# Optimization experiments

Hardware: AMD Instinct MI355X
Metric: run time of the kernel (lower is better)

The kernel has to match this reference:

```python
import jax, jax.numpy as jnp
import numpy as np

NX, NU, N, BATCH = 64, 32, 32, 192
NEWTON_ITERS = 2  # fixed outer Newton iterations (original loops to kkt_tol)


def setup_inputs() -> dict:
    key = jax.random.key(0)
    ks = jax.random.split(key, 8)
    x0 = jax.random.normal(ks[0], (BATCH, NX), jnp.float32)
    x = 0.1 * jax.random.normal(ks[1], (N + 1, BATCH, NX), jnp.float32)
    u = 0.1 * jax.random.normal(ks[2], (N, BATCH, NU), jnp.float32)
    lmd = jnp.zeros((N + 1, BATCH, NX), jnp.float32)
    # linear dynamics x+ = A x + Bm u (stable-ish A)
    A = 0.9 * jnp.eye(NX, dtype=jnp.float32) + (0.1 / np.sqrt(NX)) * jax.random.normal(ks[3], (NX, NX), jnp.float32)
    Bm = jax.random.normal(ks[4], (NX, NU), jnp.float32) / np.sqrt(NX)
    # quadratic cost weights (symmetric PD)
    Cx = jax.random.normal(ks[5], (NX, NX), jnp.float32) / np.sqrt(NX)
    Qx = Cx @ Cx.T + 0.1 * jnp.eye(NX, dtype=jnp.float32)
    Cu = jax.random.normal(ks[6], (NU, NU), jnp.float32) / np.sqrt(NU)
    Ru = Cu @ Cu.T + jnp.eye(NU, dtype=jnp.float32)
    Cf = jax.random.normal(ks[7], (NX, NX), jnp.float32) / np.sqrt(NX)
    Qf = Cf @ Cf.T + 0.1 * jnp.eye(NX, dtype=jnp.float32)
    return {"x0": x0, "x": x, "u": u, "lmd": lmd, "A": A, "Bm": Bm, "Qx": Qx, "Ru": Ru, "Qf": Qf}


def _eval_kkt(x0, x, u, lmd, A, Bm, Qx, Ru, Qf):
    # KKT residuals of the LQ OCP (GaussNewton; vectorized over stages s and batch b)
    x0res = x[0] - x0                                                   # [B,nx]
    xs = x[:-1]                                                         # [N,B,nx]
    xres = jnp.einsum('ij,sbj->sbi', A, xs) + jnp.einsum('ij,sbj->sbi', Bm, u) - x[1:]
    lx = jnp.einsum('ij,sbj->sbi', Qx, xs) + jnp.einsum('ji,sbj->sbi', A, lmd[1:]) - lmd[:-1]
    lu = jnp.einsum('ij,sbj->sbi', Ru, u) + jnp.einsum('ji,sbj->sbi', Bm, lmd[1:])
    lxN = jnp.einsum('ij,bj->bi', Qf, x[-1]) - lmd[-1]                  # terminal gradient residual
    return x0res, xres, lx, lu, lxN


def _riccati(x0res, xres, lx, lu, lxN, A, Bm, Qx, Ru, Qf):
    B_, nx = x0res.shape
    PN = jnp.broadcast_to(Qf, (B_, nx, nx))

    def bwd(carry, inp):
        P, p = carry
        lx_i, lu_i, xres_i = inp
        PA = jnp.einsum('bij,jk->bik', P, A)
        PB = jnp.einsum('bij,jk->bik', P, Bm)
        Qxx = Qx[None] + jnp.einsum('ji,bjk->bik', A, PA)
        Quu = Ru[None] + jnp.einsum('ji,bjk->bik', Bm, PB)
        Qxu = jnp.einsum('ji,bjk->bik', A, PB)
        w = jnp.einsum('bij,bj->bi', P, xres_i) + p
        qx = lx_i + jnp.einsum('ji,bj->bi', A, w)
        qu = lu_i + jnp.einsum('ji,bj->bi', Bm, w)
        rhs = jnp.concatenate([jnp.swapaxes(Qxu, 1, 2), qu[..., None]], axis=2)
        sol = -jnp.linalg.solve(Quu, rhs)
        K, k = sol[..., :nx], sol[..., nx]
        Pn = Qxx + jnp.einsum('bxi,biy->bxy', Qxu, K)
        Pn = 0.5 * (Pn + jnp.swapaxes(Pn, 1, 2))
        pn = qx + jnp.einsum('bxi,bi->bx', Qxu, k)
        return (Pn, pn), (Pn, pn, K, k)

    (_, _), (Ps, ps, Ks, ks) = jax.lax.scan(bwd, (PN, lxN), (lx, lu, xres), reverse=True)
    Ps = jnp.concatenate([Ps, PN[None]], axis=0)   # [N+1,B,nx,nx]
    ps = jnp.concatenate([ps, lxN[None]], axis=0)  # [N+1,B,nx]

    def fwd(dx, inp):
        K, k, xres_i = inp
        du = jnp.einsum('bux,bx->bu', K, dx) + k
        dxn = jnp.einsum('ij,bj->bi', A, dx) + jnp.einsum('ij,bj->bi', Bm, du) + xres_i
        return dxn, (dx, du)

    dxN, (dxs, dus) = jax.lax.scan(fwd, -x0res, (Ks, ks, xres))
    dxs = jnp.concatenate([dxs, dxN[None]], axis=0)
    dlmd = jnp.einsum('sbij,sbj->sbi', Ps, dxs) + ps
    return dxs, dus, dlmd


def _solve(x0, x, u, lmd, A, Bm, Qx, Ru, Qf):
    for _ in range(NEWTON_ITERS):
        x0res, xres, lx, lu, lxN = _eval_kkt(x0, x, u, lmd, A, Bm, Qx, Ru, Qf)
        dx, du, dlmd = _riccati(x0res, xres, lx, lu, lxN, A, Bm, Qx, Ru, Qf)
        x = x + dx
        u = u + du
        lmd = lmd + dlmd
    return x, u, lmd


def reference(x0, x, u, lmd, A, Bm, Qx, Ru, Qf):
    # returns the optimized control trajectory u* [N,B,nu]
    return _solve(x0, x, u, lmd, A, Bm, Qx, Ru, Qf)[1]
```

## Files before the change

### kernel.cpp

```cpp
#include <hip/hip_runtime.h>

#define DEV __device__ __forceinline__

constexpr int NX = 64, NU = 32, NH = 32, NB = 192;

constexpr int WS_P  = 0;
constexpr int WS_QI = WS_P  + (NH + 1) * NX * NX;
constexpr int WS_X  = WS_QI + NH * NU * NU;
constexpr int WS_K  = WS_X  + NH * NX * NU;

typedef __attribute__((ext_vector_type(8))) short bf16x8;
typedef __attribute__((ext_vector_type(4))) float f32x4;
typedef __attribute__((ext_vector_type(4))) unsigned short us4;

constexpr int LVL_M2T = 96 * 72 * 2;
constexpr int LVL_P   = 64 * 72 * 2;
constexpr int LVL_TT  = 96 * 72 * 2;
constexpr int LVL_XU  = 64 * 40 * 2;
constexpr int LVL_KT  = 64 * 40 * 2;
constexpr int LVL_QI  = 32 * 40 * 2;
constexpr int oM2T = 0;
constexpr int oP   = oM2T + 3 * LVL_M2T;
constexpr int oTT  = oP   + 3 * LVL_P;
constexpr int oXU  = oTT  + 3 * LVL_TT;
constexpr int oKT  = oXU  + 2 * LVL_XU;
constexpr int oQI  = oKT  + 2 * LVL_KT;
constexpr int oQXX = oQI  + 2 * LVL_QI;
constexpr int SMEMB = oQXX + 64 * 68 * 4;

DEV unsigned short bfh(float x) {
  unsigned u = __float_as_uint(x);
  return (unsigned short)((u + 0x7FFFu + ((u >> 16) & 1u)) >> 16);
}
DEV float bf2f(unsigned short h) { return __uint_as_float(((unsigned)h) << 16); }
DEV void split3(float x, unsigned short& h, unsigned short& m, unsigned short& l) {
  h = bfh(x); float r1 = x - bf2f(h);
  m = bfh(r1); float r2 = r1 - bf2f(m);
  l = bfh(r2);
}
DEV float4 ld4(const float* p) { return *reinterpret_cast<const float4*>(p); }
DEV void   st4(float* p, float4 v) { *reinterpret_cast<float4*>(p) = v; }
DEV void st4_nt(float* p, f32x4 v) {
  __builtin_nontemporal_store(v, (f32x4*)p);
}
DEV float  dot4(float4 a, float4 b) {
  return fmaf(a.x, b.x, fmaf(a.y, b.y, fmaf(a.z, b.z, a.w * b.w)));
}
DEV void fma4(float4& a, float s, float4 b) {
  a.x = fmaf(s, b.x, a.x); a.y = fmaf(s, b.y, a.y);
  a.z = fmaf(s, b.z, a.z); a.w = fmaf(s, b.w, a.w);
}
DEV void fma8(float* acc, float s, float4 b0, float4 b1) {
  acc[0] = fmaf(s, b0.x, acc[0]); acc[1] = fmaf(s, b0.y, acc[1]);
  acc[2] = fmaf(s, b0.z, acc[2]); acc[3] = fmaf(s, b0.w, acc[3]);
  acc[4] = fmaf(s, b1.x, acc[4]); acc[5] = fmaf(s, b1.y, acc[5]);
  acc[6] = fmaf(s, b1.z, acc[6]); acc[7] = fmaf(s, b1.w, acc[7]);
}

#define MFMA16(a, b, c) __builtin_amdgcn_mfma_f32_16x16x32_bf16(a, b, c, 0, 0, 0)

DEV f32x4 prod33(const char* A, int ao, int LA, const char* B, int bo, int LB,
                 f32x4 acc) {
  const bf16x8 a0 = *(const bf16x8*)(A + ao);
  const bf16x8 a1 = *(const bf16x8*)(A + LA + ao);
  const bf16x8 a2 = *(const bf16x8*)(A + 2 * LA + ao);
  const bf16x8 b0 = *(const bf16x8*)(B + bo);
  const bf16x8 b1 = *(const bf16x8*)(B + LB + bo);
  const bf16x8 b2 = *(const bf16x8*)(B + 2 * LB + bo);
  acc = MFMA16(a1, b1, acc);
  acc = MFMA16(a2, b0, acc);
  acc = MFMA16(a0, b2, acc);
  acc = MFMA16(a1, b0, acc);
  acc = MFMA16(a0, b1, acc);
  acc = MFMA16(a0, b0, acc);
  return acc;
}
DEV f32x4 prod22(const char* A, int ao, int LA, const char* B, int bo, int LB,
                 f32x4 acc) {
  const bf16x8 a0 = *(const bf16x8*)(A + ao);
  const bf16x8 a1 = *(const bf16x8*)(A + LA + ao);
  const bf16x8 b0 = *(const bf16x8*)(B + bo);
  const bf16x8 b1 = *(const bf16x8*)(B + LB + bo);
  acc = MFMA16(a1, b0, acc);
  acc = MFMA16(a0, b1, acc);
  acc = MFMA16(a0, b0, acc);
  return acc;
}
DEV void st_pack3(char* base, int lvl, int el, f32x4 v) {
  us4 h, m, l;
#pragma unroll
  for (int r = 0; r < 4; ++r) {
    unsigned short hh, mm, ll; split3(v[r], hh, mm, ll);
    h[r] = (short)hh; m[r] = (short)mm; l[r] = (short)ll;
  }
  *(us4*)(base + el * 2) = h;
  *(us4*)(base + lvl + el * 2) = m;
  *(us4*)(base + 2 * lvl + el * 2) = l;
}
DEV void st_pack2(char* base, int lvl, int el, f32x4 v) {
  us4 h, l;
#pragma unroll
  for (int r = 0; r < 4; ++r) {
    const unsigned short hh = bfh(v[r]);
    h[r] = (short)hh;
    l[r] = (short)bfh(v[r] - bf2f(hh));
  }
  *(us4*)(base + el * 2) = h;
  *(us4*)(base + lvl + el * 2) = l;
}

DEV void producer(char* smem, const float* Ag, const float* Bg,
                  const float* Qxg, const float* Rug, const float* Qfg,
                  float* ws) {
  const int t = threadIdx.x, lane = t & 63, wv = t >> 6;
  const int l15 = lane & 15, l4 = lane >> 4;

  char* M2T = smem + oM2T;
  char* Pp  = smem + oP;
  char* TT  = smem + oTT;
  char* XU  = smem + oXU;
  char* KT  = smem + oKT;
  char* QI  = smem + oQI;
  float* QXX = (float*)(smem + oQXX);
  float* QUU = (float*)(smem + oQXX);

  float* gP  = ws + WS_P;
  float* gQI = ws + WS_QI;
  float* gX  = ws + WS_X;
  float* gK  = ws + WS_K;
  int* flags = (int*)(ws + WS_P);

  for (int idx = t; idx < 96 * 64; idx += 512) {
    const int j = idx >> 6, m = idx & 63;
    const float v = (j < 64) ? Ag[m * 64 + j] : Bg[m * 32 + (j - 64)];
    unsigned short h, mi, lo; split3(v, h, mi, lo);
    const int eo = (j * 72 + m) * 2;
    *(unsigned short*)(M2T + eo) = h;
    *(unsigned short*)(M2T + LVL_M2T + eo) = mi;
    *(unsigned short*)(M2T + 2 * LVL_M2T + eo) = lo;
  }
  for (int idx = t; idx < 64 * 64; idx += 512) {
    const int r = idx >> 6, c = idx & 63;
    const float v = Qfg[idx];
    unsigned short h, mi, lo; split3(v, h, mi, lo);
    const int eo = (r * 72 + c) * 2;
    *(unsigned short*)(Pp + eo) = h;
    *(unsigned short*)(Pp + LVL_P + eo) = mi;
    *(unsigned short*)(Pp + 2 * LVL_P + eo) = lo;
    __builtin_nontemporal_store(v, gP + 32 * 4096 + idx);
  }
  __syncthreads();

  for (int s = NH - 1; s >= 0; --s) {
    {
      const int mT = wv >> 1, jT = 4 + (wv & 1);
      f32x4 acc = {0.f, 0.f, 0.f, 0.f};
#pragma unroll
      for (int kp = 0; kp < 2; ++kp) {
        const int ao = ((mT * 16 + l15) * 72 + kp * 32 + l4 * 8) * 2;
        const int bo = ((jT * 16 + l15) * 72 + kp * 32 + l4 * 8) * 2;
        acc = prod33(Pp, ao, LVL_P, M2T, bo, LVL_M2T, acc);
      }
      st_pack3(TT, LVL_TT, (jT * 16 + l15) * 72 + mT * 16 + l4 * 4, acc);
    }
    __syncthreads();

    if (wv < 4) {
      const int uA = wv >> 1, uB = wv & 1;
      f32x4 acc = {0.f, 0.f, 0.f, 0.f};
#pragma unroll
      for (int kp = 0; kp < 2; ++kp) {
        const int ao = (((4 + uA) * 16 + l15) * 72 + kp * 32 + l4 * 8) * 2;
        const int bo = ((64 + uB * 16 + l15) * 72 + kp * 32 + l4 * 8) * 2;
        acc = prod33(TT, ao, LVL_TT, M2T, bo, LVL_M2T, acc);
      }
      const int c = uB * 16 + l15, u0 = uA * 16 + l4 * 4;
      const float4 rv = ld4(Rug + c * 32 + u0);
      QUU[c * 36 + u0 + 0] = acc[0] + rv.x;
      QUU[c * 36 + u0 + 1] = acc[1] + rv.y;
      QUU[c * 36 + u0 + 2] = acc[2] + rv.z;
      QUU[c * 36 + u0 + 3] = acc[3] + rv.w;
    } else {
      for (int q = wv - 4; q < 8; q += 4) {
        const int uT = q & 1, xT = q >> 1;
        f32x4 acc = {0.f, 0.f, 0.f, 0.f};
#pragma unroll
        for (int kp = 0; kp < 2; ++kp) {
          const int ao = (((4 + uT) * 16 + l15) * 72 + kp * 32 + l4 * 8) * 2;
          const int bo = ((xT * 16 + l15) * 72 + kp * 32 + l4 * 8) * 2;
          acc = prod33(TT, ao, LVL_TT, M2T, bo, LVL_M2T, acc);
        }
        const int x = xT * 16 + l15, u0 = uT * 16 + l4 * 4;
        st_pack2(XU, LVL_XU, x * 40 + u0, acc);
        st4_nt(gX + s * 2048 + x * 32 + u0, acc);
      }
    }
    __syncthreads();

    if (wv == 0) {
      const int i = lane & 31, h = lane >> 5;
      float W[16];
#pragma unroll
      for (int r = 0; r < 16; ++r) W[r] = QUU[i * 36 + h * 16 + r];
#pragma unroll
      for (int j = 0; j < 32; ++j) {
        const int jh = j >> 4, jr = j & 15;
        const float d = __shfl(W[jr], j | (jh << 5));
        const float pinv = 1.0f / d;
        const float f = __shfl(W[jr], i | (jh << 5));
        float pr[16];
#pragma unroll
        for (int r = 0; r < 16; ++r) pr[r] = __shfl(W[r], j | (h << 5));
        float nw[16];
        if (i == j) {
#pragma unroll
          for (int r = 0; r < 16; ++r) nw[r] = pr[r] * pinv;
          if (h == jh) nw[jr] = pinv;
        } else {
          const float g = f * pinv;
#pragma unroll
          for (int r = 0; r < 16; ++r) nw[r] = fmaf(-g, pr[r], W[r]);
          if (h == jh) nw[jr] = -g;
        }
#pragma unroll
        for (int r = 0; r < 16; ++r) W[r] = nw[r];
      }
#pragma unroll
      for (int q = 0; q < 4; ++q) {
        f32x4 o = {W[4 * q], W[4 * q + 1], W[4 * q + 2], W[4 * q + 3]};
        st4_nt(gQI + s * 1024 + i * 32 + h * 16 + 4 * q, o);
        us4 hh, ll;
#pragma unroll
        for (int r = 0; r < 4; ++r) {
          const unsigned short hv = bfh(W[4 * q + r]);
          hh[r] = (short)hv;
          ll[r] = (short)bfh(W[4 * q + r] - bf2f(hv));
        }
        *(us4*)(QI + (i * 40 + h * 16 + 4 * q) * 2) = hh;
        *(us4*)(QI + LVL_QI + (i * 40 + h * 16 + 4 * q) * 2) = ll;
      }
    } else {
      for (int tt = wv - 1; tt < 16; tt += 7) {
        const int mT = tt & 3, jT = tt >> 2;
        f32x4 acc = {0.f, 0.f, 0.f, 0.f};
#pragma unroll
        for (int kp = 0; kp < 2; ++kp) {
          const int ao = ((mT * 16 + l15) * 72 + kp * 32 + l4 * 8) * 2;
          const int bo = ((jT * 16 + l15) * 72 + kp * 32 + l4 * 8) * 2;
          acc = prod33(Pp, ao, LVL_P, M2T, bo, LVL_M2T, acc);
        }
        st_pack3(TT, LVL_TT, (jT * 16 + l15) * 72 + mT * 16 + l4 * 4, acc);
      }
    }
    __syncthreads();

    if (wv < 2) {
      for (int tt = wv; tt < 8; tt += 2) {
        const int mT = tt & 1, xT = tt >> 1;
        f32x4 acc = {0.f, 0.f, 0.f, 0.f};
        const int ao = ((mT * 16 + l15) * 40 + l4 * 8) * 2;
        const int bo = ((xT * 16 + l15) * 40 + l4 * 8) * 2;
        acc = prod22(QI, ao, LVL_QI, XU, bo, LVL_XU, acc);
        const int x = xT * 16 + l15, m0 = mT * 16 + l4 * 4;
#pragma unroll
        for (int r = 0; r < 4; ++r)
          __builtin_nontemporal_store(-acc[r], gK + s * 2048 + (m0 + r) * 64 + x);
        st_pack2(KT, LVL_KT, x * 40 + m0, acc);
      }
    } else {
      for (int tt = wv - 2; tt < 16; tt += 6) {
        const int jT = tt >> 2, iT = tt & 3;
        f32x4 acc = {0.f, 0.f, 0.f, 0.f};
#pragma unroll
        for (int kp = 0; kp < 2; ++kp) {
          const int ao = ((jT * 16 + l15) * 72 + kp * 32 + l4 * 8) * 2;
          const int bo = ((iT * 16 + l15) * 72 + kp * 32 + l4 * 8) * 2;
          acc = prod33(TT, ao, LVL_TT, M2T, bo, LVL_M2T, acc);
        }
        const int c = iT * 16 + l15, j0 = jT * 16 + l4 * 4;
        const float4 q = ld4(Qxg + c * 64 + j0);
        QXX[c * 68 + j0 + 0] = acc[0] + q.x;
        QXX[c * 68 + j0 + 1] = acc[1] + q.y;
        QXX[c * 68 + j0 + 2] = acc[2] + q.z;
        QXX[c * 68 + j0 + 3] = acc[3] + q.w;
      }
    }
    __syncthreads();

    if (t == 0) {
      __threadfence();
      __hip_atomic_store(flags + s, 1, __ATOMIC_RELEASE, __HIP_MEMORY_SCOPE_AGENT);
    }

    if (s > 0) {
      for (int tt = wv; tt < 16; tt += 8) {
        const int iT = tt & 3, jT = tt >> 2;
        f32x4 acc = {0.f, 0.f, 0.f, 0.f};
        const int ao = ((iT * 16 + l15) * 40 + l4 * 8) * 2;
        const int bo = ((jT * 16 + l15) * 40 + l4 * 8) * 2;
        acc = prod22(XU, ao, LVL_XU, KT, bo, LVL_KT, acc);
        const int j = jT * 16 + l15, i0 = iT * 16 + l4 * 4;
        f32x4 pv;
#pragma unroll
        for (int r = 0; r < 4; ++r) {
          pv[r] = QXX[(i0 + r) * 68 + j] - acc[r];
          __builtin_nontemporal_store(pv[r], gP + s * 4096 + (i0 + r) * 64 + j);
        }
        st_pack3(Pp, LVL_P, j * 72 + i0, pv);
      }
    }
    __syncthreads();
  }
}

DEV void consumer(float* lds, int b, const float* x0g, const float* xg,
                  const float* ug, const float* lg, const float* Ag,
                  const float* Bg, const float* Qxg, const float* Rug,
                  const float* Qfg, float* ws, float* outp) {
  const int t = threadIdx.x;
  const float* gP  = ws + WS_P;
  const float* gQI = ws + WS_QI;
  const float* gX  = ws + WS_X;
  const float* gK  = ws + WS_K;
  int* flags = (int*)(ws + WS_P);

  float* sx   = lds;
  float* sl   = lds + 2112;
  float* su   = lds + 4224;
  float* sAT  = lds;
  float* xres = lds + 5248;
  float* lxs  = lds + 7296;
  float* lus  = lds + 9344;
  float* kv   = lds + 10368;
  float* swv  = lds + 11392;
  float* sqv  = lds + 11456;
  float* sduv = lds + 11488;
  float* sdxv = lds + 11520;

  for (int idx = t; idx < (NH + 1) * NX; idx += 512) {
    const int s = idx >> 6, i = idx & 63;
    sx[idx] = xg[(s * NB + b) * NX + i];
    sl[idx] = lg[(s * NB + b) * NX + i];
  }
  for (int idx = t; idx < NH * NU; idx += 512) {
    const int s = idx >> 5, j = idx & 31;
    su[idx] = ug[(s * NB + b) * NU + j];
  }
  __syncthreads();

  if (t < 256) {
    const int s = t >> 3, i0 = (t & 7) * 8;
    float accx[8], accl[8];
#pragma unroll
    for (int ii = 0; ii < 8; ++ii) {
      accx[ii] = -sx[(s + 1) * NX + i0 + ii];
      accl[ii] = -sl[s * NX + i0 + ii];
    }
#pragma unroll 2
    for (int k0 = 0; k0 < NX; k0 += 4) {
      const float4 xv = ld4(sx + s * NX + k0);
#pragma unroll
      for (int ii = 0; ii < 8; ++ii) {
        accx[ii] += dot4(ld4(Ag + (i0 + ii) * NX + k0), xv);
        accl[ii] += dot4(ld4(Qxg + (i0 + ii) * NX + k0), xv);
      }
    }
#pragma unroll 2
    for (int k0 = 0; k0 < NU; k0 += 4) {
      const float4 uv = ld4(su + s * NU + k0);
#pragma unroll
      for (int ii = 0; ii < 8; ++ii)
        accx[ii] += dot4(ld4(Bg + (i0 + ii) * NU + k0), uv);
    }
#pragma unroll 4
    for (int k = 0; k < NX; ++k) {
      const float lv = sl[(s + 1) * NX + k];
      fma8(accl, lv, ld4(Ag + k * NX + i0), ld4(Ag + k * NX + i0 + 4));
    }
#pragma unroll
    for (int ii = 0; ii < 8; ++ii) {
      xres[s * NX + i0 + ii] = accx[ii];
      lxs[s * NX + i0 + ii] = accl[ii];
    }
  }
  if (t < 256) {
    const int s = t >> 3, j0 = (t & 7) * 4;
    float4 acc = {0, 0, 0, 0};
#pragma unroll 2
    for (int k0 = 0; k0 < NU; k0 += 4) {
      const float4 uv = ld4(su + s * NU + k0);
      acc.x += dot4(ld4(Rug + (j0 + 0) * NU + k0), uv);
      acc.y += dot4(ld4(Rug + (j0 + 1) * NU + k0), uv);
      acc.z += dot4(ld4(Rug + (j0 + 2) * NU + k0), uv);
      acc.w += dot4(ld4(Rug + (j0 + 3) * NU + k0), uv);
    }
#pragma unroll 4
    for (int k = 0; k < NX; ++k) {
      const float lv = sl[(s + 1) * NX + k];
      fma4(acc, lv, ld4(Bg + k * NU + j0));
    }
    lus[s * NU + j0 + 0] = acc.x; lus[s * NU + j0 + 1] = acc.y;
    lus[s * NU + j0 + 2] = acc.z; lus[s * NU + j0 + 3] = acc.w;
  }

  float p_i = 0.0f, dx_i = 0.0f;
  if (t < 64) {
    const int i = t;
    float acc = -sl[NH * NX + i];
#pragma unroll 4
    for (int k0 = 0; k0 < NX; k0 += 4)
      acc += dot4(ld4(Qfg + i * NX + k0), ld4(sx + NH * NX + k0));
    p_i = acc;
    dx_i = x0g[b * NX + i] - sx[i];
  }
  __syncthreads();

  for (int idx = t; idx < NX * NX / 4; idx += 512) {
    const int k = idx >> 4, i4 = (idx & 15) * 4;
    const float4 a4 = ld4(Ag + k * NX + i4);
    sAT[(i4 + 0) * 68 + k] = a4.x;
    sAT[(i4 + 1) * 68 + k] = a4.y;
    sAT[(i4 + 2) * 68 + k] = a4.z;
    sAT[(i4 + 3) * 68 + k] = a4.w;
  }
  __syncthreads();

  if (t >= 64) return;

  const int i = t;
  const int j = t & 31;
  const int hh = t >> 5;

  for (int s = NH - 1; s >= 0; --s) {
    while (__hip_atomic_load(flags + s, __ATOMIC_RELAXED,
                             __HIP_MEMORY_SCOPE_AGENT) == 0)
      __builtin_amdgcn_s_sleep(4);
    (void)__hip_atomic_load(flags + s, __ATOMIC_ACQUIRE,
                            __HIP_MEMORY_SCOPE_AGENT);

    const float* Pr = gP + (s + 1) * NX * NX + i * NX;
    const float* xr = xres + s * NX;
    float w = p_i;
#pragma unroll
    for (int k0 = 0; k0 < NX; k0 += 16) {
      w += dot4(ld4(Pr + k0),      ld4(xr + k0));
      w += dot4(ld4(Pr + k0 + 4),  ld4(xr + k0 + 4));
      w += dot4(ld4(Pr + k0 + 8),  ld4(xr + k0 + 8));
      w += dot4(ld4(Pr + k0 + 12), ld4(xr + k0 + 12));
    }
    swv[i] = w;

    float qx = lxs[s * NX + i];
#pragma unroll
    for (int k0 = 0; k0 < NX; k0 += 16) {
      qx += dot4(ld4(sAT + i * 68 + k0),      ld4(swv + k0));
      qx += dot4(ld4(sAT + i * 68 + k0 + 4),  ld4(swv + k0 + 4));
      qx += dot4(ld4(sAT + i * 68 + k0 + 8),  ld4(swv + k0 + 8));
      qx += dot4(ld4(sAT + i * 68 + k0 + 12), ld4(swv + k0 + 12));
    }

    float qa = 0.0f;
    const int kb = hh * 32;
#pragma unroll 8
    for (int kk = 0; kk < 32; ++kk)
      qa = fmaf(Bg[(kb + kk) * NU + j], swv[kb + kk], qa);
    qa += __shfl_xor(qa, 32);
    const float qu = qa + lus[s * NU + j];
    if (hh == 0) sqv[j] = qu;

    const float* Qr = gQI + s * NU * NU + j * NU + hh * 16;
    float ka = dot4(ld4(Qr),      ld4(sqv + hh * 16))
             + dot4(ld4(Qr + 4),  ld4(sqv + hh * 16 + 4))
             + dot4(ld4(Qr + 8),  ld4(sqv + hh * 16 + 8))
             + dot4(ld4(Qr + 12), ld4(sqv + hh * 16 + 12));
    ka += __shfl_xor(ka, 32);
    if (hh == 0) kv[s * NU + j] = -ka;

    const float* Xs = gX + s * 2048 + i * 32;
    float pp = qx;
#pragma unroll
    for (int m0 = 0; m0 < NU; m0 += 4)
      pp += dot4(ld4(Xs + m0), ld4(kv + s * NU + m0));
    p_i = pp;
  }

  sdxv[i] = dx_i;
  for (int s = 0; s < NH; ++s) {
    const float* Kr = gK + s * NU * NX + j * NX + hh * 32;
    const float* dxh = sdxv + hh * 32;
    float da = 0.0f;
#pragma unroll
    for (int k0 = 0; k0 < 32; k0 += 16) {
      da += dot4(ld4(Kr + k0),      ld4(dxh + k0));
      da += dot4(ld4(Kr + k0 + 4),  ld4(dxh + k0 + 4));
      da += dot4(ld4(Kr + k0 + 8),  ld4(dxh + k0 + 8));
      da += dot4(ld4(Kr + k0 + 12), ld4(dxh + k0 + 12));
    }
    da += __shfl_xor(da, 32);
    const float du = da + kv[s * NU + j];
    if (hh == 0) {
      const int gi = (s * NB + b) * NU + j;
      outp[gi] = ug[gi] + du;
      sduv[j] = du;
    }

    float nxv = xres[s * NX + i];
    const float* Ar = Ag + i * NX;
#pragma unroll
    for (int k0 = 0; k0 < NX; k0 += 4)
      nxv += dot4(ld4(Ar + k0), ld4(sdxv + k0));
    const float* Br = Bg + i * NU;
#pragma unroll
    for (int m0 = 0; m0 < NU; m0 += 4)
      nxv += dot4(ld4(Br + m0), ld4(sduv + m0));
    sdxv[i] = nxv;
  }
}

__global__ void k_zero(float* ws) {
  if (threadIdx.x < 64) ((int*)(ws + WS_P))[threadIdx.x] = 0;
}

__global__ __launch_bounds__(512) void k_fused(
    const float* __restrict__ x0g, const float* __restrict__ xg,
    const float* __restrict__ ug, const float* __restrict__ lg,
    const float* __restrict__ Ag, const float* __restrict__ Bg,
    const float* __restrict__ Qxg, const float* __restrict__ Rug,
    const float* __restrict__ Qfg, float* __restrict__ ws,
    float* __restrict__ outp) {
  __shared__ __align__(16) char smem[SMEMB];
  if (blockIdx.x == 0)
    producer(smem, Ag, Bg, Qxg, Rug, Qfg, ws);
  else
    consumer((float*)smem, blockIdx.x - 1, x0g, xg, ug, lg, Ag, Bg, Qxg, Rug,
             Qfg, ws, outp);
}

extern "C" void kernel_launch(void* const* d_in, const int* in_sizes, int n_in,
                              void* d_out, int out_size, void* d_ws, size_t ws_size,
                              hipStream_t stream) {
  const float* x0  = (const float*)d_in[0];
  const float* x   = (const float*)d_in[1];
  const float* u   = (const float*)d_in[2];
  const float* lmd = (const float*)d_in[3];
  const float* A   = (const float*)d_in[4];
  const float* Bm  = (const float*)d_in[5];
  const float* Qx  = (const float*)d_in[6];
  const float* Ru  = (const float*)d_in[7];
  const float* Qf  = (const float*)d_in[8];
  float* ws  = (float*)d_ws;
  float* out = (float*)d_out;

  hipLaunchKernelGGL(k_zero, dim3(1), dim3(64), 0, stream, ws);
  hipLaunchKernelGGL(k_fused, dim3(NB + 1), dim3(512), 0, stream,
                     x0, x, u, lmd, A, Bm, Qx, Ru, Qf, ws, out);
}
```

Measured before the change: 386.7 us.

## Publish per-stage flag earlier and add final completion flag for forward pass

The per-stage release flag now fires after the QI/X stage instead of after the K/QXX stage, so consumers can start their backward recursion sooner. A new flag 32 signals completion of the whole producer loop, and consumers wait on it before the forward rollout that reads K. The 2-level bf16 split for XU, KT and QI is replaced by a 3-level split, and TT is shrunk to only the used rows. The extra split level adds MFMA work and LDS traffic in exchange for accuracy. The earlier signal aims to overlap consumer work with the producer's K and P updates.

```diff
diff --git a/kernel.cpp b/kernel.cpp
--- a/kernel.cpp
+++ b/kernel.cpp
@@ -15,7 +15,7 @@
 
 constexpr int LVL_M2T = 96 * 72 * 2;
 constexpr int LVL_P   = 64 * 72 * 2;
-constexpr int LVL_TT  = 96 * 72 * 2;
+constexpr int LVL_TT  = 64 * 72 * 2;
 constexpr int LVL_XU  = 64 * 40 * 2;
 constexpr int LVL_KT  = 64 * 40 * 2;
 constexpr int LVL_QI  = 32 * 40 * 2;
@@ -23,9 +23,9 @@
 constexpr int oP   = oM2T + 3 * LVL_M2T;
 constexpr int oTT  = oP   + 3 * LVL_P;
 constexpr int oXU  = oTT  + 3 * LVL_TT;
-constexpr int oKT  = oXU  + 2 * LVL_XU;
-constexpr int oQI  = oKT  + 2 * LVL_KT;
-constexpr int oQXX = oQI  + 2 * LVL_QI;
+constexpr int oKT  = oXU  + 3 * LVL_XU;
+constexpr int oQI  = oKT  + 3 * LVL_KT;
+constexpr int oQXX = oQI  + 3 * LVL_QI;
 constexpr int SMEMB = oQXX + 64 * 68 * 4;
 
 DEV unsigned short bfh(float x) {
@@ -75,17 +75,6 @@
   acc = MFMA16(a0, b0, acc);
   return acc;
 }
-DEV f32x4 prod22(const char* A, int ao, int LA, const char* B, int bo, int LB,
-                 f32x4 acc) {
-  const bf16x8 a0 = *(const bf16x8*)(A + ao);
-  const bf16x8 a1 = *(const bf16x8*)(A + LA + ao);
-  const bf16x8 b0 = *(const bf16x8*)(B + bo);
-  const bf16x8 b1 = *(const bf16x8*)(B + LB + bo);
-  acc = MFMA16(a1, b0, acc);
-  acc = MFMA16(a0, b1, acc);
-  acc = MFMA16(a0, b0, acc);
-  return acc;
-}
 DEV void st_pack3(char* base, int lvl, int el, f32x4 v) {
   us4 h, m, l;
 #pragma unroll
@@ -96,17 +85,6 @@
   *(us4*)(base + el * 2) = h;
   *(us4*)(base + lvl + el * 2) = m;
   *(us4*)(base + 2 * lvl + el * 2) = l;
-}
-DEV void st_pack2(char* base, int lvl, int el, f32x4 v) {
-  us4 h, l;
-#pragma unroll
-  for (int r = 0; r < 4; ++r) {
-    const unsigned short hh = bfh(v[r]);
-    h[r] = (short)hh;
-    l[r] = (short)bfh(v[r] - bf2f(hh));
-  }
-  *(us4*)(base + el * 2) = h;
-  *(us4*)(base + lvl + el * 2) = l;
 }
 
 DEV void producer(char* smem, const float* Ag, const float* Bg,
@@ -153,15 +131,15 @@
 
   for (int s = NH - 1; s >= 0; --s) {
     {
-      const int mT = wv >> 1, jT = 4 + (wv & 1);
+      const int mT = wv >> 1, vT = wv & 1;
       f32x4 acc = {0.f, 0.f, 0.f, 0.f};
 #pragma unroll
       for (int kp = 0; kp < 2; ++kp) {
         const int ao = ((mT * 16 + l15) * 72 + kp * 32 + l4 * 8) * 2;
-        const int bo = ((jT * 16 + l15) * 72 + kp * 32 + l4 * 8) * 2;
+        const int bo = (((4 + vT) * 16 + l15) * 72 + kp * 32 + l4 * 8) * 2;
         acc = prod33(Pp, ao, LVL_P, M2T, bo, LVL_M2T, acc);
       }
-      st_pack3(TT, LVL_TT, (jT * 16 + l15) * 72 + mT * 16 + l4 * 4, acc);
+      st_pack3(TT, LVL_TT, (vT * 16 + l15) * 72 + mT * 16 + l4 * 4, acc);
     }
     __syncthreads();
 
@@ -170,7 +148,7 @@
       f32x4 acc = {0.f, 0.f, 0.f, 0.f};
 #pragma unroll
       for (int kp = 0; kp < 2; ++kp) {
-        const int ao = (((4 + uA) * 16 + l15) * 72 + kp * 32 + l4 * 8) * 2;
+        const int ao = ((uA * 16 + l15) * 72 + kp * 32 + l4 * 8) * 2;
         const int bo = ((64 + uB * 16 + l15) * 72 + kp * 32 + l4 * 8) * 2;
         acc = prod33(TT, ao, LVL_TT, M2T, bo, LVL_M2T, acc);
       }
@@ -186,12 +164,12 @@
         f32x4 acc = {0.f, 0.f, 0.f, 0.f};
 #pragma unroll
         for (int kp = 0; kp < 2; ++kp) {
-          const int ao = (((4 + uT) * 16 + l15) * 72 + kp * 32 + l4 * 8) * 2;
+          const int ao = ((uT * 16 + l15) * 72 + kp * 32 + l4 * 8) * 2;
           const int bo = ((xT * 16 + l15) * 72 + kp * 32 + l4 * 8) * 2;
           acc = prod33(TT, ao, LVL_TT, M2T, bo, LVL_M2T, acc);
         }
         const int x = xT * 16 + l15, u0 = uT * 16 + l4 * 4;
-        st_pack2(XU, LVL_XU, x * 40 + u0, acc);
+        st_pack3(XU, LVL_XU, x * 40 + u0, acc);
         st4_nt(gX + s * 2048 + x * 32 + u0, acc);
       }
     }
@@ -229,15 +207,7 @@
       for (int q = 0; q < 4; ++q) {
         f32x4 o = {W[4 * q], W[4 * q + 1], W[4 * q + 2], W[4 * q + 3]};
         st4_nt(gQI + s * 1024 + i * 32 + h * 16 + 4 * q, o);
-        us4 hh, ll;
-#pragma unroll
-        for (int r = 0; r < 4; ++r) {
-          const unsigned short hv = bfh(W[4 * q + r]);
-          hh[r] = (short)hv;
-          ll[r] = (short)bfh(W[4 * q + r] - bf2f(hv));
-        }
-        *(us4*)(QI + (i * 40 + h * 16 + 4 * q) * 2) = hh;
-        *(us4*)(QI + LVL_QI + (i * 40 + h * 16 + 4 * q) * 2) = ll;
+        st_pack3(QI, LVL_QI, i * 40 + h * 16 + 4 * q, o);
       }
     } else {
       for (int tt = wv - 1; tt < 16; tt += 7) {
@@ -254,18 +224,23 @@
     }
     __syncthreads();
 
+    if (t == 0) {
+      __threadfence();
+      __hip_atomic_store(flags + s, 1, __ATOMIC_RELEASE, __HIP_MEMORY_SCOPE_AGENT);
+    }
+
     if (wv < 2) {
       for (int tt = wv; tt < 8; tt += 2) {
         const int mT = tt & 1, xT = tt >> 1;
         f32x4 acc = {0.f, 0.f, 0.f, 0.f};
         const int ao = ((mT * 16 + l15) * 40 + l4 * 8) * 2;
         const int bo = ((xT * 16 + l15) * 40 + l4 * 8) * 2;
-        acc = prod22(QI, ao, LVL_QI, XU, bo, LVL_XU, acc);
+        acc = prod33(QI, ao, LVL_QI, XU, bo, LVL_XU, acc);
         const int x = xT * 16 + l15, m0 = mT * 16 + l4 * 4;
 #pragma unroll
         for (int r = 0; r < 4; ++r)
           __builtin_nontemporal_store(-acc[r], gK + s * 2048 + (m0 + r) * 64 + x);
-        st_pack2(KT, LVL_KT, x * 40 + m0, acc);
+        st_pack3(KT, LVL_KT, x * 40 + m0, acc);
       }
     } else {
       for (int tt = wv - 2; tt < 16; tt += 6) {
@@ -287,18 +262,13 @@
     }
     __syncthreads();
 
-    if (t == 0) {
-      __threadfence();
-      __hip_atomic_store(flags + s, 1, __ATOMIC_RELEASE, __HIP_MEMORY_SCOPE_AGENT);
-    }
-
     if (s > 0) {
       for (int tt = wv; tt < 16; tt += 8) {
         const int iT = tt & 3, jT = tt >> 2;
         f32x4 acc = {0.f, 0.f, 0.f, 0.f};
         const int ao = ((iT * 16 + l15) * 40 + l4 * 8) * 2;
         const int bo = ((jT * 16 + l15) * 40 + l4 * 8) * 2;
-        acc = prod22(XU, ao, LVL_XU, KT, bo, LVL_KT, acc);
+        acc = prod33(XU, ao, LVL_XU, KT, bo, LVL_KT, acc);
         const int j = jT * 16 + l15, i0 = iT * 16 + l4 * 4;
         f32x4 pv;
 #pragma unroll
@@ -310,6 +280,11 @@
       }
     }
     __syncthreads();
+  }
+
+  if (t == 0) {
+    __threadfence();
+    __hip_atomic_store(flags + 32, 1, __ATOMIC_RELEASE, __HIP_MEMORY_SCOPE_AGENT);
   }
 }
 
@@ -483,6 +458,12 @@
       pp += dot4(ld4(Xs + m0), ld4(kv + s * NU + m0));
     p_i = pp;
   }
+
+  while (__hip_atomic_load(flags + 32, __ATOMIC_RELAXED,
+                           __HIP_MEMORY_SCOPE_AGENT) == 0)
+    __builtin_amdgcn_s_sleep(4);
+  (void)__hip_atomic_load(flags + 32, __ATOMIC_ACQUIRE,
+                          __HIP_MEMORY_SCOPE_AGENT);
 
   sdxv[i] = dx_i;
   for (int s = 0; s < NH; ++s) {
```

Result: slower. 412.7 us (+6.7%).
